# Kernel tuning notes

Measured on AMD Instinct MI355X. Metric: run time of the kernel, lower is better.

The kernel has to match this reference:

```python
import jax, jax.numpy as jnp
import numpy as np

N = 100000   # n_nodes
E = 500000   # n_edges
EH = 256     # e_hidden
RH = 128     # r_hidden
R = 1000     # n_relations (rel.max()+1, pinned in setup)


def _seg_softmax(logits, seg, num_segments):
    # numerically-stable softmax grouped by segment id
    m = jax.ops.segment_max(logits, seg, num_segments=num_segments)
    ex = jnp.exp(logits - m[seg])
    s = jax.ops.segment_sum(ex, seg, num_segments=num_segments)
    return ex / s[seg]


def setup_inputs() -> dict:
    key = jax.random.key(0)
    ks = jax.random.split(key, 14)
    s_e = 1.0 / np.sqrt(EH)
    s_r = 1.0 / np.sqrt(RH)
    x_e = jax.random.normal(ks[0], (N, EH), dtype=jnp.float32)
    edge_index = jax.random.randint(ks[1], (2, E), 0, N, dtype=jnp.int32)
    rel = jax.random.randint(ks[2], (E,), 0, R, dtype=jnp.int32).at[0].set(R - 1)
    rel_all = jax.random.randint(ks[3], (E,), 0, R, dtype=jnp.int32)
    return {
        "x_e": x_e,
        "edge_index": edge_index,
        "rel": rel,
        "rel_all": rel_all,
        "w_h": jax.random.normal(ks[4], (EH, RH), dtype=jnp.float32) * s_e,
        "w_t": jax.random.normal(ks[5], (EH, RH), dtype=jnp.float32) * s_e,
        "a_h1": jax.random.normal(ks[6], (RH,), dtype=jnp.float32) * s_r,
        "a_h2": jax.random.normal(ks[7], (RH,), dtype=jnp.float32) * s_r,
        "a_t1": jax.random.normal(ks[8], (RH,), dtype=jnp.float32) * s_r,
        "a_t2": jax.random.normal(ks[9], (RH,), dtype=jnp.float32) * s_r,
        "r_h_w": jax.random.normal(ks[10], (RH, RH), dtype=jnp.float32) * s_r,
        "r_h_b": jax.random.normal(ks[11], (RH,), dtype=jnp.float32) * s_r,
        "r_t_w": jax.random.normal(ks[12], (RH, RH), dtype=jnp.float32) * s_r,
        "r_t_b": jax.random.normal(ks[13], (RH,), dtype=jnp.float32) * s_r,
    }


def reference(x_e, edge_index, rel, rel_all, w_h, w_t, a_h1, a_h2, a_t1, a_t2,
              r_h_w, r_h_b, r_t_w, r_t_b):
    h_idx, t_idx = edge_index[0], edge_index[1]
    x_r_h = x_e @ w_h          # [N, RH]
    x_r_t = x_e @ w_t          # [N, RH]
    # per-node attention scalars, gathered per edge
    e1 = (x_r_h @ a_h1)[h_idx] + (x_r_t @ a_h2)[t_idx]   # [E]
    e2 = (x_r_h @ a_t1)[h_idx] + (x_r_t @ a_t2)[t_idx]   # [E]
    alpha_h = _seg_softmax(jax.nn.leaky_relu(e1, 0.01), rel, R)
    alpha_t = _seg_softmax(jax.nn.leaky_relu(e2, 0.01), rel, R)
    # sparse.mm(adj, M) == segment-sum over edges of alpha[e] * M[node[e]] into row rel[e]
    msg_h = x_r_h @ r_h_w + r_h_b + x_r_h                 # [N, RH]
    msg_t = x_r_t @ r_t_w + r_t_b + x_r_t                 # [N, RH]
    out_h = jax.ops.segment_sum(alpha_h[:, None] * msg_h[h_idx], rel, num_segments=R)
    out_t = jax.ops.segment_sum(alpha_t[:, None] * msg_t[t_idx], rel, num_segments=R)
    return out_h + out_t                                   # [R, RH]
```

## Files before the change

kernel.cpp:

```cpp
#include <hip/hip_runtime.h>
#include <hip/hip_bf16.h>
#include <math.h>


#define EHD 256
#define RHD 128
#define RMAX 1024
#define SCHUNK 2048
#define SEGMAX 4096

typedef __attribute__((ext_vector_type(8))) short short8;
typedef __attribute__((ext_vector_type(4))) float f32x4;

__device__ __forceinline__ short f2bf(float x) {
    __hip_bfloat16 b = __float2bfloat16(x);
    return *reinterpret_cast<short*>(&b);
}
__device__ __forceinline__ float bfu(unsigned int u) {
    return __uint_as_float(u << 16);
}
__device__ __forceinline__ float leaky(float x) { return x > 0.f ? x : 0.01f * x; }
__device__ __forceinline__ int xswz(int row, int col) {
    return col ^ ((row & 7) << 3);
}

__global__ __launch_bounds__(256) void k_prep(const float* __restrict__ src,
                                              short* __restrict__ dst,
                                              int K, int Nc)
{
    __shared__ float t[32][33];
    const int k0 = blockIdx.x * 32, n0 = blockIdx.y * 32;
    const int tr = threadIdx.x >> 3, tc = (threadIdx.x & 7) << 2;
    float4 v = *reinterpret_cast<const float4*>(src + (size_t)(k0 + tr) * Nc + n0 + tc);
    t[tr][tc + 0] = v.x; t[tr][tc + 1] = v.y;
    t[tr][tc + 2] = v.z; t[tr][tc + 3] = v.w;
    __syncthreads();
    short* o = dst + (size_t)(n0 + tr) * K + k0 + tc;
    o[0] = f2bf(t[tc + 0][tr]); o[1] = f2bf(t[tc + 1][tr]);
    o[2] = f2bf(t[tc + 2][tr]); o[3] = f2bf(t[tc + 3][tr]);
}

__global__ __launch_bounds__(256, 4) void k_fused(
    const float* __restrict__ xe,
    const short* __restrict__ whT, const short* __restrict__ wtT,
    const float* __restrict__ ah1, const float* __restrict__ ah2,
    const float* __restrict__ at1, const float* __restrict__ at2,
    float2* __restrict__ sA, float2* __restrict__ sB,
    short* __restrict__ xrh, short* __restrict__ xrt, int N)
{
    __shared__ __align__(16) union {
        short Bs[2][2][128][32];
        short Xs[2][64][128];
    } u;

    const int tid = threadIdx.x;
    const int w = tid >> 6, l = tid & 63;
    const int ln = l & 15, lk = l >> 4;
    const int m0 = blockIdx.x * 64;
    const int orow = (w << 4) + (lk << 2);

    f32x4 acch[8], acct[8];
#pragma unroll
    for (int c = 0; c < 8; c++) {
        acch[c] = (f32x4){0.f, 0.f, 0.f, 0.f};
        acct[c] = (f32x4){0.f, 0.f, 0.f, 0.f};
    }

    const int arow = m0 + (w << 4) + ln;
    const int aclamp = min(arow, N - 1);
    const float* abase = xe + (size_t)aclamp * EHD + (lk << 3);
    short* BsFlat = &u.Bs[0][0][0][0];

    const int Rl = l >> 2, kc = l & 3;

    auto stage = [&](int buf, int kt) {
#pragma unroll
        for (int i = 0; i < 4; i++) {
            const int j = (w << 2) + i;
            const int R = (j << 4) + Rl;
            const int mat = R >> 7, row = R & 127;
            const short* g = (mat ? wtT : whT) + (size_t)row * EHD + kt + (kc << 3);
            __builtin_amdgcn_global_load_lds(
                (const __attribute__((address_space(1))) void*)g,
                (__attribute__((address_space(3))) void*)(BsFlat + (buf << 13) + (j << 9)),
                16, 0, 0);
        }
    };

    float4 a0 = *reinterpret_cast<const float4*>(abase);
    float4 a1 = *reinterpret_cast<const float4*>(abase + 4);
    stage(0, 0);

#pragma unroll
    for (int s = 0; s < 8; s++) {
        const int kt = s << 5;
        __syncthreads();
        if (s < 7) stage((s + 1) & 1, kt + 32);
        short8 af;
        af[0] = f2bf(a0.x); af[1] = f2bf(a0.y); af[2] = f2bf(a0.z); af[3] = f2bf(a0.w);
        af[4] = f2bf(a1.x); af[5] = f2bf(a1.y); af[6] = f2bf(a1.z); af[7] = f2bf(a1.w);
        if (s < 7) {
            a0 = *reinterpret_cast<const float4*>(abase + kt + 32);
            a1 = *reinterpret_cast<const float4*>(abase + kt + 36);
        }
        const int b = s & 1;
#pragma unroll
        for (int c = 0; c < 8; c++) {
            short8 bh = *reinterpret_cast<const short8*>(&u.Bs[b][0][(c << 4) + ln][lk << 3]);
            short8 bt = *reinterpret_cast<const short8*>(&u.Bs[b][1][(c << 4) + ln][lk << 3]);
            acch[c] = __builtin_amdgcn_mfma_f32_16x16x32_bf16(af, bh, acch[c], 0, 0, 0);
            acct[c] = __builtin_amdgcn_mfma_f32_16x16x32_bf16(af, bt, acct[c], 0, 0, 0);
        }
    }
    __syncthreads();

    float p1[4] = {0,0,0,0}, p2[4] = {0,0,0,0}, p3[4] = {0,0,0,0}, p4[4] = {0,0,0,0};
#pragma unroll
    for (int c = 0; c < 8; c++) {
        const int col = (c << 4) + ln;
        const float wa1 = ah1[col], wa2 = ah2[col], wa3 = at1[col], wa4 = at2[col];
#pragma unroll
        for (int r = 0; r < 4; r++) {
            const float vh = acch[c][r], vt = acct[c][r];
            p1[r] = fmaf(vh, wa1, p1[r]);
            p3[r] = fmaf(vh, wa3, p3[r]);
            p2[r] = fmaf(vt, wa2, p2[r]);
            p4[r] = fmaf(vt, wa4, p4[r]);
            const int row = orow + r;
            const int cs = xswz(row, col);
            u.Xs[0][row][cs] = f2bf(vh);
            u.Xs[1][row][cs] = f2bf(vt);
        }
    }
#pragma unroll
    for (int off = 1; off < 16; off <<= 1) {
#pragma unroll
        for (int r = 0; r < 4; r++) {
            p1[r] += __shfl_xor(p1[r], off);
            p2[r] += __shfl_xor(p2[r], off);
            p3[r] += __shfl_xor(p3[r], off);
            p4[r] += __shfl_xor(p4[r], off);
        }
    }
    if (ln == 0) {
#pragma unroll
        for (int r = 0; r < 4; r++) {
            const int grow = m0 + orow + r;
            if (grow < N) {
                sA[grow] = make_float2(p1[r], p3[r]);
                sB[grow] = make_float2(p2[r], p4[r]);
            }
        }
    }
    __syncthreads();
#pragma unroll
    for (int it = 0; it < 8; it++) {
        const int idx = tid + (it << 8);
        const int mat = idx >> 10;
        const int rem = idx & 1023;
        const int row = rem >> 4;
        const int ch  = rem & 15;
        const int grow = m0 + row;
        if (grow < N) {
            const int cs = (ch << 3) ^ ((row & 7) << 3);
            short8 v = *reinterpret_cast<const short8*>(&u.Xs[mat][row][cs]);
            short* dst = (mat ? xrt : xrh) + (size_t)grow * RHD + (ch << 3);
            *reinterpret_cast<short8*>(dst) = v;
        }
    }
}

__global__ __launch_bounds__(256) void k_hist(const int* __restrict__ rel,
                                              int* __restrict__ counts, int R, int E)
{
    __shared__ int cnt[RMAX];
    for (int i = threadIdx.x; i < R; i += 256) cnt[i] = 0;
    __syncthreads();
    for (int e = blockIdx.x * 256 + threadIdx.x; e < E; e += gridDim.x * 256)
        atomicAdd(&cnt[rel[e]], 1);
    __syncthreads();
    for (int i = threadIdx.x; i < R; i += 256) {
        int v = cnt[i];
        if (v) atomicAdd(&counts[i], v);
    }
}

__global__ __launch_bounds__(1024) void k_scan(
    const int* __restrict__ counts, int* __restrict__ starts,
    int* __restrict__ cursor, int R, int E)
{
    __shared__ int buf[2][1024];
    int t = threadIdx.x;
    int v = (t < R) ? counts[t] : 0;
    buf[0][t] = v;
    int cur = 0;
    for (int off = 1; off < 1024; off <<= 1) {
        __syncthreads();
        int x = buf[cur][t];
        if (t >= off) x += buf[cur][t - off];
        buf[cur ^ 1][t] = x;
        cur ^= 1;
    }
    __syncthreads();
    int incl = buf[cur][t];
    if (t < R) { starts[t] = incl - v; cursor[t] = incl - v; }
    if (t == 0) starts[R] = E;
}

__global__ __launch_bounds__(256) void k_scatter(
    const int* __restrict__ rel, int* __restrict__ cursor,
    const int* __restrict__ eh, const int* __restrict__ et,
    const float2* __restrict__ sA, const float2* __restrict__ sB,
    int2* __restrict__ rec1, int2* __restrict__ rec2, int R, int E)
{
    __shared__ int lcnt[RMAX];
    __shared__ int lbase[RMAX];
    const int tid = threadIdx.x;
    const int base = blockIdx.x * SCHUNK;
    const int nE = min(SCHUNK, E - base);
    for (int i = tid; i < R; i += 256) lcnt[i] = 0;
    __syncthreads();
    for (int i = tid; i < nE; i += 256) atomicAdd(&lcnt[rel[base + i]], 1);
    __syncthreads();
    for (int r = tid; r < R; r += 256) {
        int c = lcnt[r];
        lbase[r] = c ? atomicAdd(&cursor[r], c) : 0;
        lcnt[r] = 0;
    }
    __syncthreads();
    for (int i = tid; i < nE; i += 256) {
        const int e = base + i;
        const int r = rel[e];
        const int off = atomicAdd(&lcnt[r], 1);
        const int pos = lbase[r] + off;
        const int h = eh[e], t = et[e];
        const float2 va = sA[h];
        const float2 vb = sB[t];
        const float e1 = leaky(va.x + vb.x);
        const float e2 = leaky(va.y + vb.y);
        rec1[pos] = make_int2(h, __float_as_int(e1));
        rec2[pos] = make_int2(t, __float_as_int(e2));
    }
}

__global__ __launch_bounds__(512) void k_rel(
    const int* __restrict__ starts,
    const int2* __restrict__ rec1, const int2* __restrict__ rec2,
    const short* __restrict__ xrh, const short* __restrict__ xrt,
    float* __restrict__ y, int R)
{
    const int r = blockIdx.x;
    const int side = blockIdx.y;
    const int start = starts[r], end = starts[r + 1];
    const int len = end - start;
    if (len <= 0) return;
    const int tid = threadIdx.x;
    const int2* __restrict__ rc = (side ? rec2 : rec1) + start;
    const unsigned short* __restrict__ mb =
        reinterpret_cast<const unsigned short*>(side ? xrt : xrh);

    __shared__ float red[16];
    __shared__ int   lnode[SEGMAX];
    __shared__ float lal[SEGMAX];
    __shared__ float part[8][128];

    const int slot = tid >> 6;
    const int jj = tid & 63;
    float a0 = 0.f, a1 = 0.f;

    if (len <= SEGMAX) {
        float m = -INFINITY;
        for (int i = tid; i < len; i += 512) {
            int2 v = rc[i];
            lnode[i] = v.x;
            float e = __int_as_float(v.y);
            lal[i] = e;
            m = fmaxf(m, e);
        }
#pragma unroll
        for (int off = 32; off > 0; off >>= 1) m = fmaxf(m, __shfl_xor(m, off));
        if ((tid & 63) == 0) red[slot] = m;
        __syncthreads();
        m = fmaxf(fmaxf(fmaxf(red[0], red[1]), fmaxf(red[2], red[3])),
                  fmaxf(fmaxf(red[4], red[5]), fmaxf(red[6], red[7])));
        __syncthreads();

        float sum = 0.f;
        for (int i = tid; i < len; i += 512) {
            float x = __expf(lal[i] - m);
            lal[i] = x;
            sum += x;
        }
#pragma unroll
        for (int off = 32; off > 0; off >>= 1) sum += __shfl_xor(sum, off);
        if ((tid & 63) == 0) red[8 + slot] = sum;
        __syncthreads();
        sum = ((red[8] + red[9]) + (red[10] + red[11]))
            + ((red[12] + red[13]) + (red[14] + red[15]));
        const float inv = 1.f / sum;

        int q = slot;
        for (; q + 24 < len; q += 32) {
            const float w0 = lal[q] * inv;       const int n0 = lnode[q];
            const float w1 = lal[q + 8] * inv;   const int n1 = lnode[q + 8];
            const float w2 = lal[q + 16] * inv;  const int n2 = lnode[q + 16];
            const float w3 = lal[q + 24] * inv;  const int n3 = lnode[q + 24];
            const unsigned int v0 =
                *reinterpret_cast<const unsigned int*>(mb + (size_t)n0 * RHD + (jj << 1));
            const unsigned int v1 =
                *reinterpret_cast<const unsigned int*>(mb + (size_t)n1 * RHD + (jj << 1));
            const unsigned int v2 =
                *reinterpret_cast<const unsigned int*>(mb + (size_t)n2 * RHD + (jj << 1));
            const unsigned int v3 =
                *reinterpret_cast<const unsigned int*>(mb + (size_t)n3 * RHD + (jj << 1));
            a0 = fmaf(w0, bfu(v0 & 0xffffu), a0);
            a1 = fmaf(w0, bfu(v0 >> 16), a1);
            a0 = fmaf(w1, bfu(v1 & 0xffffu), a0);
            a1 = fmaf(w1, bfu(v1 >> 16), a1);
            a0 = fmaf(w2, bfu(v2 & 0xffffu), a0);
            a1 = fmaf(w2, bfu(v2 >> 16), a1);
            a0 = fmaf(w3, bfu(v3 & 0xffffu), a0);
            a1 = fmaf(w3, bfu(v3 >> 16), a1);
        }
        for (; q < len; q += 8) {
            const float w0 = lal[q] * inv;
            const int   n0 = lnode[q];
            const unsigned int v0 =
                *reinterpret_cast<const unsigned int*>(mb + (size_t)n0 * RHD + (jj << 1));
            a0 = fmaf(w0, bfu(v0 & 0xffffu), a0);
            a1 = fmaf(w0, bfu(v0 >> 16), a1);
        }
    } else {
        float m = -INFINITY;
        for (int i = tid; i < len; i += 512) m = fmaxf(m, __int_as_float(rc[i].y));
#pragma unroll
        for (int off = 32; off > 0; off >>= 1) m = fmaxf(m, __shfl_xor(m, off));
        if ((tid & 63) == 0) red[slot] = m;
        __syncthreads();
        m = fmaxf(fmaxf(fmaxf(red[0], red[1]), fmaxf(red[2], red[3])),
                  fmaxf(fmaxf(red[4], red[5]), fmaxf(red[6], red[7])));
        __syncthreads();

        float sum = 0.f;
        for (int i = tid; i < len; i += 512) sum += __expf(__int_as_float(rc[i].y) - m);
#pragma unroll
        for (int off = 32; off > 0; off >>= 1) sum += __shfl_xor(sum, off);
        if ((tid & 63) == 0) red[8 + slot] = sum;
        __syncthreads();
        sum = ((red[8] + red[9]) + (red[10] + red[11]))
            + ((red[12] + red[13]) + (red[14] + red[15]));
        const float inv = 1.f / sum;

        for (int c0 = 0; c0 < len; c0 += 512) {
            __syncthreads();
            int i = c0 + tid;
            if (i < len) {
                int2 v = rc[i];
                lal[tid] = __expf(__int_as_float(v.y) - m) * inv;
                lnode[tid] = v.x;
            }
            __syncthreads();
            const int nc = min(512, len - c0);
            for (int q = slot; q < nc; q += 8) {
                const float wq = lal[q];
                const int n = lnode[q];
                const unsigned int v =
                    *reinterpret_cast<const unsigned int*>(mb + (size_t)n * RHD + (jj << 1));
                a0 = fmaf(wq, bfu(v & 0xffffu), a0);
                a1 = fmaf(wq, bfu(v >> 16), a1);
            }
        }
    }

    part[slot][(jj << 1) + 0] = a0;
    part[slot][(jj << 1) + 1] = a1;
    __syncthreads();
    if (tid < 128) {
        float v = ((part[0][tid] + part[1][tid]) + (part[2][tid] + part[3][tid]))
                + ((part[4][tid] + part[5][tid]) + (part[6][tid] + part[7][tid]));
        y[((size_t)side * R + r) * RHD + tid] = v;
    }
}

__global__ __launch_bounds__(128) void k_out(
    const float* __restrict__ y,
    const float* __restrict__ rhw, const float* __restrict__ rtw,
    const float* __restrict__ rhb, const float* __restrict__ rtb,
    const int* __restrict__ starts,
    float* __restrict__ out, int R)
{
    const int r = blockIdx.x;
    const int j = threadIdx.x;
    __shared__ float ph[RHD], pt[RHD];
    ph[j] = y[(size_t)r * RHD + j];
    pt[j] = y[((size_t)R + r) * RHD + j];
    __syncthreads();
    float acc = ph[j] + pt[j];
    if (starts[r + 1] > starts[r]) acc += rhb[j] + rtb[j];
    float a = 0.f;
#pragma unroll 8
    for (int k = 0; k < RHD; k++) {
        a = fmaf(ph[k], rhw[k * RHD + j], a);
        a = fmaf(pt[k], rtw[k * RHD + j], a);
    }
    out[(size_t)r * RHD + j] = acc + a;
}

extern "C" void kernel_launch(void* const* d_in, const int* in_sizes, int n_in,
                              void* d_out, int out_size, void* d_ws, size_t ws_size,
                              hipStream_t stream)
{
    const float* xe  = (const float*)d_in[0];
    const int*  eidx = (const int*)d_in[1];
    const int*  rel  = (const int*)d_in[2];
    const float* wh  = (const float*)d_in[4];
    const float* wt  = (const float*)d_in[5];
    const float* ah1 = (const float*)d_in[6];
    const float* ah2 = (const float*)d_in[7];
    const float* at1 = (const float*)d_in[8];
    const float* at2 = (const float*)d_in[9];
    const float* rhw = (const float*)d_in[10];
    const float* rhb = (const float*)d_in[11];
    const float* rtw = (const float*)d_in[12];
    const float* rtb = (const float*)d_in[13];
    float* out = (float*)d_out;

    const int N = in_sizes[0] / EHD;
    const int E = in_sizes[2];
    const int R = out_size / RHD;
    const int* eh = eidx;
    const int* et = eidx + E;

    char* ws = (char*)d_ws;
    size_t off = 0;
    auto alloc = [&](size_t bytes) -> void* {
        void* p = ws + off;
        off = (off + bytes + 255) & ~(size_t)255;
        return p;
    };
    short* xrh   = (short*)alloc((size_t)N * RHD * sizeof(short));
    short* xrt   = (short*)alloc((size_t)N * RHD * sizeof(short));
    short* whT   = (short*)alloc((size_t)RHD * EHD * sizeof(short));
    short* wtT   = (short*)alloc((size_t)RHD * EHD * sizeof(short));
    float* y     = (float*)alloc((size_t)2 * R * RHD * sizeof(float));
    float2* sA   = (float2*)alloc((size_t)N * sizeof(float2));
    float2* sB   = (float2*)alloc((size_t)N * sizeof(float2));
    int* counts  = (int*)alloc((size_t)R * sizeof(int));
    int* starts  = (int*)alloc((size_t)(R + 1) * sizeof(int));
    int* cursor  = (int*)alloc((size_t)R * sizeof(int));
    int2* rec1   = (int2*)alloc((size_t)E * sizeof(int2));
    int2* rec2   = (int2*)alloc((size_t)E * sizeof(int2));
    (void)ws_size; (void)n_in;

    hipMemsetAsync(counts, 0, (size_t)R * sizeof(int), stream);
    hipMemsetAsync(y, 0, (size_t)2 * R * RHD * sizeof(float), stream);

    k_prep<<<dim3(EHD / 32, RHD / 32), 256, 0, stream>>>(wh, whT, EHD, RHD);
    k_prep<<<dim3(EHD / 32, RHD / 32), 256, 0, stream>>>(wt, wtT, EHD, RHD);

    k_fused<<<(N + 63) / 64, 256, 0, stream>>>(
        xe, whT, wtT, ah1, ah2, at1, at2,
        sA, sB, xrh, xrt, N);

    k_hist<<<128, 256, 0, stream>>>(rel, counts, R, E);
    k_scan<<<1, 1024, 0, stream>>>(counts, starts, cursor, R, E);
    k_scatter<<<(E + SCHUNK - 1) / SCHUNK, 256, 0, stream>>>(
        rel, cursor, eh, et, sA, sB, rec1, rec2, R, E);
    k_rel<<<dim3(R, 2), 512, 0, stream>>>(starts, rec1, rec2, xrh, xrt, y, R);
    k_out<<<R, 128, 0, stream>>>(y, rhw, rtw, rhb, rtb, starts, out, R);
}
```

Before: 131.4 us.

## Fuse weight prep launches, fold histogram into GEMM, drop softmax max pass

```diff
diff --git a/kernel.cpp b/kernel.cpp
--- a/kernel.cpp
+++ b/kernel.cpp
@@ -6,6 +6,7 @@
 #define EHD 256
 #define RHD 128
 #define RMAX 1024
+#define HBLK 128
 #define SCHUNK 2048
 #define SEGMAX 4096
 
@@ -24,18 +25,21 @@
     return col ^ ((row & 7) << 3);
 }
 
-__global__ __launch_bounds__(256) void k_prep(const float* __restrict__ src,
-                                              short* __restrict__ dst,
-                                              int K, int Nc)
-{
+__global__ __launch_bounds__(256) void k_prep2(const float* __restrict__ wh,
+                                               const float* __restrict__ wt,
+                                               short* __restrict__ whT,
+                                               short* __restrict__ wtT)
+{
+    const float* src = blockIdx.z ? wt : wh;
+    short* dst = blockIdx.z ? wtT : whT;
     __shared__ float t[32][33];
     const int k0 = blockIdx.x * 32, n0 = blockIdx.y * 32;
     const int tr = threadIdx.x >> 3, tc = (threadIdx.x & 7) << 2;
-    float4 v = *reinterpret_cast<const float4*>(src + (size_t)(k0 + tr) * Nc + n0 + tc);
+    float4 v = *reinterpret_cast<const float4*>(src + (size_t)(k0 + tr) * RHD + n0 + tc);
     t[tr][tc + 0] = v.x; t[tr][tc + 1] = v.y;
     t[tr][tc + 2] = v.z; t[tr][tc + 3] = v.w;
     __syncthreads();
-    short* o = dst + (size_t)(n0 + tr) * K + k0 + tc;
+    short* o = dst + (size_t)(n0 + tr) * EHD + k0 + tc;
     o[0] = f2bf(t[tc + 0][tr]); o[1] = f2bf(t[tc + 1][tr]);
     o[2] = f2bf(t[tc + 2][tr]); o[3] = f2bf(t[tc + 3][tr]);
 }
@@ -46,11 +50,13 @@
     const float* __restrict__ ah1, const float* __restrict__ ah2,
     const float* __restrict__ at1, const float* __restrict__ at2,
     float2* __restrict__ sA, float2* __restrict__ sB,
-    short* __restrict__ xrh, short* __restrict__ xrt, int N)
+    short* __restrict__ xrh, short* __restrict__ xrt, int N,
+    const int* __restrict__ rel, int* __restrict__ counts, int R, int E)
 {
     __shared__ __align__(16) union {
         short Bs[2][2][128][32];
         short Xs[2][64][128];
+        int   Hs[RMAX];
     } u;
 
     const int tid = threadIdx.x;
@@ -77,8 +83,8 @@
 #pragma unroll
         for (int i = 0; i < 4; i++) {
             const int j = (w << 2) + i;
-            const int R = (j << 4) + Rl;
-            const int mat = R >> 7, row = R & 127;
+            const int Rr = (j << 4) + Rl;
+            const int mat = Rr >> 7, row = Rr & 127;
             const short* g = (mat ? wtT : whT) + (size_t)row * EHD + kt + (kc << 3);
             __builtin_amdgcn_global_load_lds(
                 (const __attribute__((address_space(1))) void*)g,
@@ -168,20 +174,18 @@
             *reinterpret_cast<short8*>(dst) = v;
         }
     }
-}
-
-__global__ __launch_bounds__(256) void k_hist(const int* __restrict__ rel,
-                                              int* __restrict__ counts, int R, int E)
-{
-    __shared__ int cnt[RMAX];
-    for (int i = threadIdx.x; i < R; i += 256) cnt[i] = 0;
-    __syncthreads();
-    for (int e = blockIdx.x * 256 + threadIdx.x; e < E; e += gridDim.x * 256)
-        atomicAdd(&cnt[rel[e]], 1);
-    __syncthreads();
-    for (int i = threadIdx.x; i < R; i += 256) {
-        int v = cnt[i];
-        if (v) atomicAdd(&counts[i], v);
+
+    if (blockIdx.x < HBLK) {
+        __syncthreads();
+        for (int i = tid; i < R; i += 256) u.Hs[i] = 0;
+        __syncthreads();
+        for (int e = blockIdx.x * 256 + tid; e < E; e += HBLK * 256)
+            atomicAdd(&u.Hs[rel[e]], 1);
+        __syncthreads();
+        for (int i = tid; i < R; i += 256) {
+            int v = u.Hs[i];
+            if (v) atomicAdd(&counts[i], v);
+        }
     }
 }
 
@@ -236,10 +240,10 @@
         const int h = eh[e], t = et[e];
         const float2 va = sA[h];
         const float2 vb = sB[t];
-        const float e1 = leaky(va.x + vb.x);
-        const float e2 = leaky(va.y + vb.y);
-        rec1[pos] = make_int2(h, __float_as_int(e1));
-        rec2[pos] = make_int2(t, __float_as_int(e2));
+        const float x1 = __expf(leaky(va.x + vb.x));
+        const float x2 = __expf(leaky(va.y + vb.y));
+        rec1[pos] = make_int2(h, __float_as_int(x1));
+        rec2[pos] = make_int2(t, __float_as_int(x2));
     }
 }
 
@@ -259,7 +263,7 @@
     const unsigned short* __restrict__ mb =
         reinterpret_cast<const unsigned short*>(side ? xrt : xrh);
 
-    __shared__ float red[16];
+    __shared__ float red[8];
     __shared__ int   lnode[SEGMAX];
     __shared__ float lal[SEGMAX];
     __shared__ float part[8][128];
@@ -269,34 +273,20 @@
     float a0 = 0.f, a1 = 0.f;
 
     if (len <= SEGMAX) {
-        float m = -INFINITY;
+        float sum = 0.f;
         for (int i = tid; i < len; i += 512) {
             int2 v = rc[i];
             lnode[i] = v.x;
-            float e = __int_as_float(v.y);
-            lal[i] = e;
-            m = fmaxf(m, e);
-        }
-#pragma unroll
-        for (int off = 32; off > 0; off >>= 1) m = fmaxf(m, __shfl_xor(m, off));
-        if ((tid & 63) == 0) red[slot] = m;
-        __syncthreads();
-        m = fmaxf(fmaxf(fmaxf(red[0], red[1]), fmaxf(red[2], red[3])),
-                  fmaxf(fmaxf(red[4], red[5]), fmaxf(red[6], red[7])));
-        __syncthreads();
-
-        float sum = 0.f;
-        for (int i = tid; i < len; i += 512) {
-            float x = __expf(lal[i] - m);
+            float x = __int_as_float(v.y);
             lal[i] = x;
             sum += x;
         }
 #pragma unroll
         for (int off = 32; off > 0; off >>= 1) sum += __shfl_xor(sum, off);
-        if ((tid & 63) == 0) red[8 + slot] = sum;
-        __syncthreads();
-        sum = ((red[8] + red[9]) + (red[10] + red[11]))
-            + ((red[12] + red[13]) + (red[14] + red[15]));
+        if ((tid & 63) == 0) red[slot] = sum;
+        __syncthreads();
+        sum = ((red[0] + red[1]) + (red[2] + red[3]))
+            + ((red[4] + red[5]) + (red[6] + red[7]));
         const float inv = 1.f / sum;
 
         int q = slot;
@@ -331,24 +321,14 @@
             a1 = fmaf(w0, bfu(v0 >> 16), a1);
         }
     } else {
-        float m = -INFINITY;
-        for (int i = tid; i < len; i += 512) m = fmaxf(m, __int_as_float(rc[i].y));
-#pragma unroll
-        for (int off = 32; off > 0; off >>= 1) m = fmaxf(m, __shfl_xor(m, off));
-        if ((tid & 63) == 0) red[slot] = m;
-        __syncthreads();
-        m = fmaxf(fmaxf(fmaxf(red[0], red[1]), fmaxf(red[2], red[3])),
-                  fmaxf(fmaxf(red[4], red[5]), fmaxf(red[6], red[7])));
-        __syncthreads();
-
         float sum = 0.f;
-        for (int i = tid; i < len; i += 512) sum += __expf(__int_as_float(rc[i].y) - m);
+        for (int i = tid; i < len; i += 512) sum += __int_as_float(rc[i].y);
 #pragma unroll
         for (int off = 32; off > 0; off >>= 1) sum += __shfl_xor(sum, off);
-        if ((tid & 63) == 0) red[8 + slot] = sum;
-        __syncthreads();
-        sum = ((red[8] + red[9]) + (red[10] + red[11]))
-            + ((red[12] + red[13]) + (red[14] + red[15]));
+        if ((tid & 63) == 0) red[slot] = sum;
+        __syncthreads();
+        sum = ((red[0] + red[1]) + (red[2] + red[3]))
+            + ((red[4] + red[5]) + (red[6] + red[7]));
         const float inv = 1.f / sum;
 
         for (int c0 = 0; c0 < len; c0 += 512) {
@@ -356,7 +336,7 @@
             int i = c0 + tid;
             if (i < len) {
                 int2 v = rc[i];
-                lal[tid] = __expf(__int_as_float(v.y) - m) * inv;
+                lal[tid] = __int_as_float(v.y) * inv;
                 lnode[tid] = v.x;
             }
             __syncthreads();
@@ -455,14 +435,12 @@
     hipMemsetAsync(counts, 0, (size_t)R * sizeof(int), stream);
     hipMemsetAsync(y, 0, (size_t)2 * R * RHD * sizeof(float), stream);
 
-    k_prep<<<dim3(EHD / 32, RHD / 32), 256, 0, stream>>>(wh, whT, EHD, RHD);
-    k_prep<<<dim3(EHD / 32, RHD / 32), 256, 0, stream>>>(wt, wtT, EHD, RHD);
+    k_prep2<<<dim3(EHD / 32, RHD / 32, 2), 256, 0, stream>>>(wh, wt, whT, wtT);
 
     k_fused<<<(N + 63) / 64, 256, 0, stream>>>(
         xe, whT, wtT, ah1, ah2, at1, at2,
-        sA, sB, xrh, xrt, N);
-
-    k_hist<<<128, 256, 0, stream>>>(rel, counts, R, E);
+        sA, sB, xrh, xrt, N, rel, counts, R, E);
+
     k_scan<<<1, 1024, 0, stream>>>(counts, starts, cursor, R, E);
     k_scatter<<<(E + SCHUNK - 1) / SCHUNK, 256, 0, stream>>>(
         rel, cursor, eh, et, sA, sB, rec1, rec2, R, E);
```

Result: faster. 122.4 us (-6.9%).
